# Kernel optimization log

Hardware: AMD Instinct MI355X
Metric: run time of the kernel (lower is better)

## Reference

```python
import math
import jax, jax.numpy as jnp
import numpy as np

P = 1024
P_R = 128
A_MIN, A_MAX = 0.01, 0.995
TAU_INIT = 64.0
EPS = 1e-06
B, T = 8, 4096


def _xavier(key, shape):
    fan_in, fan_out = shape[0], shape[1]
    lim = math.sqrt(6.0 / (fan_in + fan_out))
    return jax.random.uniform(key, shape, jnp.float32, -lim, lim)


def setup_inputs() -> dict:
    key = jax.random.key(0)
    k_t, k_f, k_vr, k_vb, k_vo, k_wl = jax.random.split(key, 6)
    a0 = math.exp(-1.0 / max(TAU_INIT, 1.0))
    logit_a0 = math.log(a0 / (1.0 - a0 + 1e-09))
    return {
        "t": jax.random.normal(k_t, (B, T, P), jnp.float32),
        "F": jax.random.uniform(k_f, (B, T, P), jnp.float32),
        "V_r": _xavier(k_vr, (P, P_R)),
        "V_b": _xavier(k_vb, (P, P_R)),
        "V_o": _xavier(k_vo, (P_R, P)),
        "W_lambda": 0.02 * jax.random.normal(k_wl, (P_R, P_R), jnp.float32),
        "b_lambda": jnp.full((P_R,), logit_a0, jnp.float32),
    }


def reference(t, F, V_r, V_b, V_o, W_lambda, b_lambda):
    t = t.astype(jnp.float32)
    F = jax.lax.stop_gradient(F.astype(jnp.float32))  # F is detached in the original
    scale = 1.0 / math.sqrt(P_R)

    # decay gates: a = clamp(sigmoid((t @ V_r) @ W_lambda + b_lambda))  -> (B,T,P_r)
    r = jnp.einsum('btp,pr->btr', t, V_r)
    a = jax.nn.sigmoid(jnp.einsum('btr,rs->bts', r, W_lambda) + b_lambda)
    a = jnp.clip(a, A_MIN, A_MAX)

    # input drive: u = (F * t) @ V_b * scale  -> (B,T,P_r)
    u = jnp.einsum('btp,pr->btr', F * t, V_b) * scale

    def step(s, inp):
        a_i, u_i = inp                      # (B,P_r)
        s = a_i * s + u_i
        denom = jnp.sqrt(jnp.mean(s * s, axis=-1, keepdims=True) + EPS)
        s = s / denom
        return s, s

    s0 = jnp.zeros((t.shape[0], P_R), jnp.float32)
    _, s_seq = jax.lax.scan(step, s0, (jnp.swapaxes(a, 0, 1), jnp.swapaxes(u, 0, 1)))
    s = jnp.swapaxes(s_seq, 0, 1)           # (B,T,P_r)

    t_tilde = jnp.einsum('btr,rp->btp', s, V_o) + t  # residual=True
    new_cache = s[:, -1, :]
    return t_tilde, new_cache
```

## Files before the change

kernel.cpp:

```cpp
#include <hip/hip_runtime.h>
#include <math.h>

#define P_DIM 1024
#define R_DIM 128
#define B_DIM 8
#define T_DIM 4096
#define NROWS (B_DIM*T_DIM)

__global__ __launch_bounds__(256, 2) void stage1_kernel(
    const float* __restrict__ tin, const float* __restrict__ Fin,
    const float* __restrict__ Vr, const float* __restrict__ Vb,
    const float* __restrict__ Wl, const float* __restrict__ bl,
    float* __restrict__ a_ws, float* __restrict__ u_ws)
{
    __shared__ float tA[32][36];
    __shared__ float tF[32][36];
    __shared__ float Bs[2][32][128];
    __shared__ float rS[32][132];

    const int tid  = threadIdx.x;
    const int c    = tid & 31;
    const int ry   = tid >> 5;
    const int row0 = blockIdx.x * 32;

    float accR[4][4] = {};
    float accU[4][4] = {};

    const int lr = tid >> 3;
    const int lk = (tid & 7) << 2;

    for (int k0 = 0; k0 < P_DIM; k0 += 32) {
        __syncthreads();
        float4 tv = *(const float4*)(tin + (long)(row0 + lr) * P_DIM + k0 + lk);
        float4 fv = *(const float4*)(Fin + (long)(row0 + lr) * P_DIM + k0 + lk);
        fv.x *= tv.x; fv.y *= tv.y; fv.z *= tv.z; fv.w *= tv.w;
        *(float4*)&tA[lr][lk] = tv;
        *(float4*)&tF[lr][lk] = fv;
#pragma unroll
        for (int i = 0; i < 4; i++) {
            int idx = tid + i * 256;
            ((float4*)&Bs[0][0][0])[idx] = ((const float4*)(Vr + (long)k0 * R_DIM))[idx];
            ((float4*)&Bs[1][0][0])[idx] = ((const float4*)(Vb + (long)k0 * R_DIM))[idx];
        }
        __syncthreads();
#pragma unroll
        for (int kk = 0; kk < 32; kk++) {
            float4 vr = *(const float4*)&Bs[0][kk][c * 4];
            float4 vb = *(const float4*)&Bs[1][kk][c * 4];
#pragma unroll
            for (int i = 0; i < 4; i++) {
                float ta = tA[ry * 4 + i][kk];
                float tf = tF[ry * 4 + i][kk];
                accR[i][0] = fmaf(ta, vr.x, accR[i][0]);
                accR[i][1] = fmaf(ta, vr.y, accR[i][1]);
                accR[i][2] = fmaf(ta, vr.z, accR[i][2]);
                accR[i][3] = fmaf(ta, vr.w, accR[i][3]);
                accU[i][0] = fmaf(tf, vb.x, accU[i][0]);
                accU[i][1] = fmaf(tf, vb.y, accU[i][1]);
                accU[i][2] = fmaf(tf, vb.z, accU[i][2]);
                accU[i][3] = fmaf(tf, vb.w, accU[i][3]);
            }
        }
    }

#pragma unroll
    for (int i = 0; i < 4; i++) {
        *(float4*)&rS[ry * 4 + i][c * 4] =
            make_float4(accR[i][0], accR[i][1], accR[i][2], accR[i][3]);
    }

    float4 bl4 = *(const float4*)(bl + c * 4);
    float z[4][4];
#pragma unroll
    for (int i = 0; i < 4; i++) { z[i][0] = bl4.x; z[i][1] = bl4.y; z[i][2] = bl4.z; z[i][3] = bl4.w; }

    for (int kc = 0; kc < R_DIM; kc += 32) {
        __syncthreads();
#pragma unroll
        for (int i2 = 0; i2 < 4; i2++) {
            int idx = tid + i2 * 256;
            ((float4*)&Bs[0][0][0])[idx] = ((const float4*)(Wl + (long)kc * R_DIM))[idx];
        }
        __syncthreads();
#pragma unroll
        for (int kk = 0; kk < 32; kk++) {
            float4 w = *(const float4*)&Bs[0][kk][c * 4];
#pragma unroll
            for (int i = 0; i < 4; i++) {
                float rv = rS[ry * 4 + i][kc + kk];
                z[i][0] = fmaf(rv, w.x, z[i][0]);
                z[i][1] = fmaf(rv, w.y, z[i][1]);
                z[i][2] = fmaf(rv, w.z, z[i][2]);
                z[i][3] = fmaf(rv, w.w, z[i][3]);
            }
        }
    }

    const float uscale = 0.08838834764831845f;
#pragma unroll
    for (int i = 0; i < 4; i++) {
        int row = row0 + ry * 4 + i;
        float4 av;
        av.x = fminf(fmaxf(1.f / (1.f + expf(-z[i][0])), 0.01f), 0.995f);
        av.y = fminf(fmaxf(1.f / (1.f + expf(-z[i][1])), 0.01f), 0.995f);
        av.z = fminf(fmaxf(1.f / (1.f + expf(-z[i][2])), 0.01f), 0.995f);
        av.w = fminf(fmaxf(1.f / (1.f + expf(-z[i][3])), 0.01f), 0.995f);
        *(float4*)(a_ws + (long)row * R_DIM + c * 4) = av;
        float4 uv = make_float4(accU[i][0] * uscale, accU[i][1] * uscale,
                                accU[i][2] * uscale, accU[i][3] * uscale);
        *(float4*)(u_ws + (long)row * R_DIM + c * 4) = uv;
    }
}

template <int CTRL, int ROW_MASK>
__device__ __forceinline__ float dpp_add(float x) {
    int xi = __float_as_int(x);
    int yi = __builtin_amdgcn_update_dpp(0, xi, CTRL, ROW_MASK, 0xf, false);
    return x + __int_as_float(yi);
}

__device__ __forceinline__ float wave64_sum(float x) {
    x = dpp_add<0xB1,  0xf>(x);
    x = dpp_add<0x4E,  0xf>(x);
    x = dpp_add<0x141, 0xf>(x);
    x = dpp_add<0x140, 0xf>(x);
    x = dpp_add<0x142, 0xa>(x);
    x = dpp_add<0x143, 0xc>(x);
    return __int_as_float(__builtin_amdgcn_readlane(__float_as_int(x), 63));
}

#define PF 16

__global__ __launch_bounds__(64) void scan_kernel(
    const float* __restrict__ a_ws, const float* __restrict__ u_ws,
    float* __restrict__ s_ws, float* __restrict__ cache_out)
{
    const int b = blockIdx.x;
    const int lane = threadIdx.x;
    const long base = (long)b * T_DIM * R_DIM + lane * 2;

    float2 ab[PF], ub[PF];
#pragma unroll
    for (int j = 0; j < PF; j++) {
        ab[j] = *(const float2*)(a_ws + base + (long)j * R_DIM);
        ub[j] = *(const float2*)(u_ws + base + (long)j * R_DIM);
    }

    float2 s = make_float2(0.f, 0.f);

    for (int i0 = 0; i0 < T_DIM; i0 += PF) {
#pragma unroll
        for (int j = 0; j < PF; j++) {
            const int i = i0 + j;
            float2 av = ab[j];
            float2 uv = ub[j];
            if (i0 + PF < T_DIM) {
                ab[j] = *(const float2*)(a_ws + base + (long)(i + PF) * R_DIM);
                ub[j] = *(const float2*)(u_ws + base + (long)(i + PF) * R_DIM);
            }
            float2 v;
            v.x = fmaf(av.x, s.x, uv.x);
            v.y = fmaf(av.y, s.y, uv.y);
            float sq = fmaf(v.x, v.x, v.y * v.y);
            float total = wave64_sum(sq);
            float inv = rsqrtf(fmaf(total, 0.0078125f, 1e-6f));
            s.x = v.x * inv;
            s.y = v.y * inv;
            *(float2*)(s_ws + base + (long)i * R_DIM) = s;
        }
    }
    *(float2*)(cache_out + b * R_DIM + lane * 2) = s;
}

__global__ __launch_bounds__(256, 2) void stage3_kernel(
    const float* __restrict__ s_ws, const float* __restrict__ Vo,
    const float* __restrict__ tin, float* __restrict__ out)
{
    __shared__ float sS[16][128];
    __shared__ float VoS[32][256];

    const int tid = threadIdx.x;
    const int cb = blockIdx.x & 3;
    const int rb = blockIdx.x >> 2;
    const int row0 = rb * 16;
    const int col0 = cb * 256;
    const int tx = tid & 63;
    const int ty = tid >> 6;

    float acc[4][4] = {};

#pragma unroll
    for (int i = 0; i < 2; i++) {
        int idx = tid + i * 256;
        ((float4*)&sS[0][0])[idx] = *(const float4*)(s_ws + (long)row0 * R_DIM + idx * 4);
    }

    for (int k0 = 0; k0 < R_DIM; k0 += 32) {
        __syncthreads();
#pragma unroll
        for (int i = 0; i < 8; i++) {
            int idx = tid + i * 256;
            int r = idx >> 6;
            int cq = idx & 63;
            *(float4*)&VoS[r][cq * 4] =
                *(const float4*)(Vo + (long)(k0 + r) * P_DIM + col0 + cq * 4);
        }
        __syncthreads();
#pragma unroll
        for (int kk = 0; kk < 32; kk++) {
            float4 w = *(const float4*)&VoS[kk][tx * 4];
#pragma unroll
            for (int i = 0; i < 4; i++) {
                float sv = sS[ty * 4 + i][k0 + kk];
                acc[i][0] = fmaf(sv, w.x, acc[i][0]);
                acc[i][1] = fmaf(sv, w.y, acc[i][1]);
                acc[i][2] = fmaf(sv, w.z, acc[i][2]);
                acc[i][3] = fmaf(sv, w.w, acc[i][3]);
            }
        }
    }

#pragma unroll
    for (int i = 0; i < 4; i++) {
        int row = row0 + ty * 4 + i;
        float4 tv = *(const float4*)(tin + (long)row * P_DIM + col0 + tx * 4);
        float4 o = make_float4(acc[i][0] + tv.x, acc[i][1] + tv.y,
                               acc[i][2] + tv.z, acc[i][3] + tv.w);
        *(float4*)(out + (long)row * P_DIM + col0 + tx * 4) = o;
    }
}

extern "C" void kernel_launch(void* const* d_in, const int* in_sizes, int n_in,
                              void* d_out, int out_size, void* d_ws, size_t ws_size,
                              hipStream_t stream) {
    const float* t  = (const float*)d_in[0];
    const float* F  = (const float*)d_in[1];
    const float* Vr = (const float*)d_in[2];
    const float* Vb = (const float*)d_in[3];
    const float* Vo = (const float*)d_in[4];
    const float* Wl = (const float*)d_in[5];
    const float* bl = (const float*)d_in[6];
    float* out = (float*)d_out;

    float* a_ws = (float*)d_ws;
    float* u_ws = a_ws + (long)NROWS * R_DIM;
    float* s_ws = u_ws + (long)NROWS * R_DIM;

    hipLaunchKernelGGL(stage1_kernel, dim3(NROWS / 32), dim3(256), 0, stream,
                       t, F, Vr, Vb, Wl, bl, a_ws, u_ws);
    hipLaunchKernelGGL(scan_kernel, dim3(B_DIM), dim3(64), 0, stream,
                       a_ws, u_ws, s_ws, out + (long)NROWS * P_DIM);
    hipLaunchKernelGGL(stage3_kernel, dim3((NROWS / 16) * 4), dim3(256), 0, stream,
                       s_ws, Vo, t, out);
}
```

Baseline: 1.123 ms.

## Break scan dependency by algebraic norm expansion and interleave a/u in workspace

Stage 1 now writes a and u interleaved per row into a 256-wide workspace, together with a precomputed per-row sum of u squared. The scan expands ||a*s+u||^2 into separate A, B and C terms so that both wave reductions depend only on the previous unnormalized state, which takes the reduction off the serial chain. It writes s back into the consumed slots of the interleaved buffer, and stage 3 reads it with the new stride. The aim is to shorten the latency-bound sequential scan and cut its separate loads, at the cost of extra reductions and possible rounding differences from the expanded norm.

New measurement: 1.130 ms. Within noise of the previous version (+0.6%).

```diff
diff --git a/kernel.cpp b/kernel.cpp
--- a/kernel.cpp
+++ b/kernel.cpp
@@ -11,7 +11,7 @@
     const float* __restrict__ tin, const float* __restrict__ Fin,
     const float* __restrict__ Vr, const float* __restrict__ Vb,
     const float* __restrict__ Wl, const float* __restrict__ bl,
-    float* __restrict__ a_ws, float* __restrict__ u_ws)
+    float* __restrict__ au_ws, float* __restrict__ usq_ws)
 {
     __shared__ float tA[32][36];
     __shared__ float tF[32][36];
@@ -105,10 +105,18 @@
         av.y = fminf(fmaxf(1.f / (1.f + expf(-z[i][1])), 0.01f), 0.995f);
         av.z = fminf(fmaxf(1.f / (1.f + expf(-z[i][2])), 0.01f), 0.995f);
         av.w = fminf(fmaxf(1.f / (1.f + expf(-z[i][3])), 0.01f), 0.995f);
-        *(float4*)(a_ws + (long)row * R_DIM + c * 4) = av;
         float4 uv = make_float4(accU[i][0] * uscale, accU[i][1] * uscale,
                                 accU[i][2] * uscale, accU[i][3] * uscale);
-        *(float4*)(u_ws + (long)row * R_DIM + c * 4) = uv;
+        float* dst = au_ws + ((long)row << 8) + c * 8;
+        *(float4*)dst       = make_float4(av.x, av.y, uv.x, uv.y);
+        *(float4*)(dst + 4) = make_float4(av.z, av.w, uv.z, uv.w);
+        float us = fmaf(uv.x, uv.x, fmaf(uv.y, uv.y, fmaf(uv.z, uv.z, uv.w * uv.w)));
+        us += __shfl_xor(us, 1);
+        us += __shfl_xor(us, 2);
+        us += __shfl_xor(us, 4);
+        us += __shfl_xor(us, 8);
+        us += __shfl_xor(us, 16);
+        if (c == 0) usq_ws[row] = us;
     }
 }
 
@@ -129,47 +137,68 @@
     return __int_as_float(__builtin_amdgcn_readlane(__float_as_int(x), 63));
 }
 
-#define PF 16
+#define PF 8
 
 __global__ __launch_bounds__(64) void scan_kernel(
-    const float* __restrict__ a_ws, const float* __restrict__ u_ws,
-    float* __restrict__ s_ws, float* __restrict__ cache_out)
+    float* __restrict__ au,
+    const float* __restrict__ usq,
+    float* __restrict__ cache_out)
 {
     const int b = blockIdx.x;
     const int lane = threadIdx.x;
-    const long base = (long)b * T_DIM * R_DIM + lane * 2;
-
-    float2 ab[PF], ub[PF];
+    const long rowbase = (long)b * T_DIM;
+    const float* usq_b = usq + rowbase;
+
+    float4 buf[PF];
+    float  cq[PF];
 #pragma unroll
     for (int j = 0; j < PF; j++) {
-        ab[j] = *(const float2*)(a_ws + base + (long)j * R_DIM);
-        ub[j] = *(const float2*)(u_ws + base + (long)j * R_DIM);
-    }
-
-    float2 s = make_float2(0.f, 0.f);
+        buf[j] = *(const float4*)(au + ((rowbase + j) << 8) + lane * 4);
+        cq[j]  = usq_b[j];
+    }
+
+    float2 v   = make_float2(0.f, 0.f);
+    float invp = 0.f;
+    float Ap = 0.f, Bp = 0.f, Cp = 0.f;
 
     for (int i0 = 0; i0 < T_DIM; i0 += PF) {
 #pragma unroll
         for (int j = 0; j < PF; j++) {
             const int i = i0 + j;
-            float2 av = ab[j];
-            float2 uv = ub[j];
-            if (i0 + PF < T_DIM) {
-                ab[j] = *(const float2*)(a_ws + base + (long)(i + PF) * R_DIM);
-                ub[j] = *(const float2*)(u_ws + base + (long)(i + PF) * R_DIM);
-            }
-            float2 v;
-            v.x = fmaf(av.x, s.x, uv.x);
-            v.y = fmaf(av.y, s.y, uv.y);
-            float sq = fmaf(v.x, v.x, v.y * v.y);
-            float total = wave64_sum(sq);
-            float inv = rsqrtf(fmaf(total, 0.0078125f, 1e-6f));
-            s.x = v.x * inv;
-            s.y = v.y * inv;
-            *(float2*)(s_ws + base + (long)i * R_DIM) = s;
-        }
-    }
-    *(float2*)(cache_out + b * R_DIM + lane * 2) = s;
+            float4 x = buf[j];
+            float  C = cq[j];
+            int ip = i + PF; if (ip > T_DIM - 1) ip = T_DIM - 1;
+            buf[j] = *(const float4*)(au + ((rowbase + ip) << 8) + lane * 4);
+            cq[j]  = usq_b[ip];
+
+            float px = x.x * v.x;
+            float py = x.y * v.y;
+            float pa = fmaf(px, px, py * py);
+            float pb = fmaf(px, x.z, py * x.w);
+            float A = wave64_sum(pa);
+            float B = wave64_sum(pb);
+
+            float tot = fmaf(invp * invp, Ap, fmaf(invp + invp, Bp, Cp));
+            tot = fmaxf(tot, 0.f);
+            float inv = rsqrtf(fmaf(tot, 0.0078125f, 1e-6f));
+
+            int iw = (i > 0) ? i - 1 : 0;
+            *(float2*)(au + ((rowbase + iw) << 8) + lane * 2) =
+                make_float2(inv * v.x, inv * v.y);
+
+            v.x = fmaf(inv, px, x.z);
+            v.y = fmaf(inv, py, x.w);
+
+            invp = inv; Ap = A; Bp = B; Cp = C;
+        }
+    }
+
+    float tot = fmaf(invp * invp, Ap, fmaf(invp + invp, Bp, Cp));
+    tot = fmaxf(tot, 0.f);
+    float inv = rsqrtf(fmaf(tot, 0.0078125f, 1e-6f));
+    float2 sfin = make_float2(inv * v.x, inv * v.y);
+    *(float2*)(au + ((rowbase + (T_DIM - 1)) << 8) + lane * 2) = sfin;
+    *(float2*)(cache_out + b * R_DIM + lane * 2) = sfin;
 }
 
 __global__ __launch_bounds__(256, 2) void stage3_kernel(
@@ -192,7 +221,10 @@
 #pragma unroll
     for (int i = 0; i < 2; i++) {
         int idx = tid + i * 256;
-        ((float4*)&sS[0][0])[idx] = *(const float4*)(s_ws + (long)row0 * R_DIM + idx * 4);
+        int r = idx >> 5;
+        int q = idx & 31;
+        *(float4*)&sS[r][q * 4] =
+            *(const float4*)(s_ws + ((long)(row0 + r) << 8) + q * 4);
     }
 
     for (int k0 = 0; k0 < R_DIM; k0 += 32) {
@@ -242,14 +274,13 @@
     const float* bl = (const float*)d_in[6];
     float* out = (float*)d_out;
 
-    float* a_ws = (float*)d_ws;
-    float* u_ws = a_ws + (long)NROWS * R_DIM;
-    float* s_ws = u_ws + (long)NROWS * R_DIM;
+    float* au_ws  = (float*)d_ws;
+    float* usq_ws = au_ws + (long)NROWS * 256;
 
     hipLaunchKernelGGL(stage1_kernel, dim3(NROWS / 32), dim3(256), 0, stream,
-                       t, F, Vr, Vb, Wl, bl, a_ws, u_ws);
+                       t, F, Vr, Vb, Wl, bl, au_ws, usq_ws);
     hipLaunchKernelGGL(scan_kernel, dim3(B_DIM), dim3(64), 0, stream,
-                       a_ws, u_ws, s_ws, out + (long)NROWS * P_DIM);
+                       au_ws, usq_ws, out + (long)NROWS * P_DIM);
     hipLaunchKernelGGL(stage3_kernel, dim3((NROWS / 16) * 4), dim3(256), 0, stream,
-                       s_ws, Vo, t, out);
-}
+                       au_ws, Vo, t, out);
+}
```
